# Performance work log

Hardware: AMD Instinct MI355X
Metric: run time of the kernel (lower is better)

## Reference

```python
import jax, jax.numpy as jnp
import numpy as np
import math

B, N, D = 64, 512, 300
MASK_VALUE = -1.0e9
LN_EPS = 1e-5


def setup_inputs() -> dict:
    key = jax.random.key(0)
    ks = jax.random.split(key, 8)
    return {
        "concepts": jax.random.normal(ks[0], (B, N, D), dtype=jnp.float32),
        "ocr_tokens": jax.random.normal(ks[1], (B, N, D), dtype=jnp.float32),
        "ocr_mask": jax.random.randint(ks[2], (B, N, 1), 0, 2, dtype=jnp.int32),
        "wq": jax.random.normal(ks[3], (D, D), dtype=jnp.float32) * (1.0 / math.sqrt(D)),
        "bq": jax.random.normal(ks[4], (D,), dtype=jnp.float32) * 0.02,
        "wk": jax.random.normal(ks[5], (D, D), dtype=jnp.float32) * (1.0 / math.sqrt(D)),
        "bk": jax.random.normal(ks[6], (D,), dtype=jnp.float32) * 0.02,
        "ln_w": jnp.ones((D,), dtype=jnp.float32),
        "ln_b": jnp.zeros((D,), dtype=jnp.float32),
    }


def _layer_norm(x, w, b):
    mu = jnp.mean(x, axis=-1, keepdims=True)
    var = jnp.mean(jnp.square(x - mu), axis=-1, keepdims=True)
    return (x - mu) * jax.lax.rsqrt(var + LN_EPS) * w + b


def reference(concepts, ocr_tokens, ocr_mask, wq, bq, wk, bk, ln_w, ln_b):
    # Q/K linear projections (torch Linear: x @ W^T + b)
    Q = jnp.einsum('bnd,ed->bne', concepts, wq) + bq      # [B,N,D]
    K = jnp.einsum('bmd,ed->bme', ocr_tokens, wk) + bk    # [B,N,D]
    # scaled attention scores over concepts x ocr tokens
    A = jnp.einsum('bne,bme->bnm', Q, K) / math.sqrt(D)   # [B,N,N]
    P = jax.nn.softmax(A, axis=-1)
    semantic = jnp.einsum('bnm,bmd->bnd', P, concepts)    # [B,N,D]
    # post-attention masked_fill (faithful to original: fill AFTER attention)
    semantic = jnp.where(ocr_mask == 0, jnp.float32(MASK_VALUE), semantic)
    out = _layer_norm(ocr_tokens + semantic, ln_w, ln_b)  # [B,N,D]
    return out
```

## Files before the change

kernel.cpp:

```cpp
#include <hip/hip_runtime.h>
#include <math.h>

#define Bb 64
#define Nn 512
#define Dd 300

typedef __attribute__((ext_vector_type(8))) short bfrag;
typedef __attribute__((ext_vector_type(4))) float f4;
typedef __attribute__((ext_vector_type(4))) unsigned u4;
typedef __attribute__((ext_vector_type(2))) unsigned u2;

union BF { unsigned u[4]; bfrag v; u4 q; };

__device__ inline unsigned bfr(float x){
    union{float f;unsigned u;}v; v.f=x;
    return (v.u + 0x7FFFu + ((v.u>>16)&1u))>>16;
}
__device__ inline unsigned pk_rne(float a, float b){ return bfr(a) | (bfr(b)<<16); }
__device__ inline unsigned pk_tr(float a, float b){
    union{float f;unsigned u;} ua, ub; ua.f=a; ub.f=b;
    return (ua.u>>16) | (ub.u & 0xFFFF0000u);
}
__device__ inline char* wadr(char* dout, unsigned f){
    return dout + (size_t)(f>>9)*1200u + 608u + (f&511u);
}
__device__ inline void async16(const char* g, char* l){
    __builtin_amdgcn_global_load_lds(
        (const __attribute__((address_space(1))) void*)g,
        (__attribute__((address_space(3))) void*)l, 16, 0, 0);
}

#define TSZ 38400
#define VOFF 19200
#define ZSZ 19200

__global__ __launch_bounds__(256)
void prep(const float* __restrict__ concepts, char* __restrict__ tiles,
          const float* __restrict__ wq, const float* __restrict__ wk,
          char* __restrict__ dout)
{
    const int bx = blockIdx.x;
    const int t  = threadIdx.x;
    if (bx < 1024) {
        const int mt = bx & 15, b = bx >> 4;
        char* vz = tiles + ((size_t)(b*16 + mt))*TSZ + VOFF;
        for (int task = t; task < 300; task += 256) {
            int m8 = task / 75, d4 = task - m8*75;
            const float* src = concepts + ((size_t)(b*Nn + mt*32 + m8*8))*Dd + d4*4;
            float4 r[8];
            #pragma unroll
            for (int i = 0; i < 8; ++i) r[i] = *(const float4*)(src + (size_t)i*Dd);
            #pragma unroll
            for (int dd = 0; dd < 4; ++dd) {
                int d = d4*4 + dd;
                float x[8];
                #pragma unroll
                for (int i = 0; i < 8; ++i)
                    x[i] = (dd==0) ? r[i].x : (dd==1) ? r[i].y : (dd==2) ? r[i].z : r[i].w;
                u4 q; q.x = pk_rne(x[0],x[1]); q.y = pk_rne(x[2],x[3]);
                      q.z = pk_rne(x[4],x[5]); q.w = pk_rne(x[6],x[7]);
                char* dst = (d < 288)
                    ? vz + (d>>4)*1024 + m8*256 + (d&15)*16
                    : vz + 18432 + m8*192 + (d-288)*16;
                *(u4*)dst = q;
            }
        }
    } else {
        const int wid = bx - 1024;
        const int xx = wid % 20, yy = wid / 20;
        const int sel = xx / 10, kc = xx % 10;
        const float* W = sel ? wk : wq;
        const int n = yy*152 + t;
        if (t < 152 && n < 304) {
            unsigned uu[16];
            #pragma unroll
            for (int j = 0; j < 16; ++j) uu[j] = 0;
            if (n < Dd) {
                const float* wr = W + (size_t)n*Dd + kc*32;
                int nv4 = (kc < 9) ? 8 : 3;
                #pragma unroll
                for (int i = 0; i < 8; ++i) {
                    if (i < nv4) {
                        float4 v = *(const float4*)(wr + i*4);
                        uu[2*i  ] = pk_rne(v.x, v.y);
                        uu[2*i+1] = pk_rne(v.z, v.w);
                    }
                }
            }
            unsigned fb = (unsigned)(sel*194560 + kc*19456 + n*16);
            #pragma unroll
            for (int g = 0; g < 4; ++g) {
                u4 q; q.x = uu[4*g+0]; q.y = uu[4*g+1]; q.z = uu[4*g+2]; q.w = uu[4*g+3];
                *(u4*)wadr(dout, fb + g*4864) = q;
            }
        }
    }
}

__global__ __launch_bounds__(256)
void proj4(const float* __restrict__ concepts, const float* __restrict__ ocr,
           const float* __restrict__ bq, const float* __restrict__ bk,
           char* __restrict__ dout, char* __restrict__ tiles)
{
    __shared__ char Wl[2][19456];
    const int t = threadIdx.x;
    const int w = t >> 6, lane = t & 63, ln = lane & 15, quad = lane >> 4;
    const int sel = blockIdx.y;
    const float* X    = sel ? ocr : concepts;
    const float* bias = sel ? bk  : bq;
    const int r0w = blockIdx.x*64 + w*16;
    const float* xr = X + (size_t)(r0w + ln)*Dd;

    const unsigned selbase = (unsigned)sel*194560u;
    #define STAGE_W(buf, kc) \
        for (int c = w; c < 19; c += 4) \
            async16((const char*)wadr(dout, selbase + (unsigned)(kc)*19456u + c*1024u + lane*16u), \
                    &Wl[buf][c*1024 + lane*16]);

    f4 acc[19];
    #pragma unroll
    for (int i = 0; i < 19; ++i) acc[i] = (f4){0.f,0.f,0.f,0.f};

    STAGE_W(0, 0);
    __syncthreads();

    for (int kc = 0; kc < 10; ++kc) {
        const int cur = kc & 1;
        if (kc < 9) { STAGE_W(1 - cur, kc + 1); }
        BF a;
        if (kc < 9) {
            float4 v0 = *(const float4*)(xr + kc*32 + quad*8);
            float4 v1 = *(const float4*)(xr + kc*32 + quad*8 + 4);
            a.u[0]=pk_tr(v0.x,v0.y); a.u[1]=pk_tr(v0.z,v0.w);
            a.u[2]=pk_tr(v1.x,v1.y); a.u[3]=pk_tr(v1.z,v1.w);
        } else {
            a.u[0]=0; a.u[1]=0; a.u[2]=0; a.u[3]=0;
            if (quad == 0) {
                float4 v0 = *(const float4*)(xr + 288);
                float4 v1 = *(const float4*)(xr + 292);
                a.u[0]=pk_tr(v0.x,v0.y); a.u[1]=pk_tr(v0.z,v0.w);
                a.u[2]=pk_tr(v1.x,v1.y); a.u[3]=pk_tr(v1.z,v1.w);
            } else if (quad == 1) {
                float4 v0 = *(const float4*)(xr + 296);
                a.u[0]=pk_tr(v0.x,v0.y); a.u[1]=pk_tr(v0.z,v0.w);
            }
        }
        #pragma unroll
        for (int nt = 0; nt < 19; ++nt) {
            BF bfv; bfv.q = *(const u4*)&Wl[cur][quad*4864 + nt*256 + ln*16];
            acc[nt] = __builtin_amdgcn_mfma_f32_16x16x32_bf16(a.v, bfv.v, acc[nt], 0,0,0);
        }
        __syncthreads();
    }

    const float QSCALE = 0.057735026918962584f;
    #pragma unroll
    for (int nt = 0; nt < 19; ++nt) {
        int e = nt*16 + ln;
        if (sel == 0) {
            #pragma unroll
            for (int reg = 0; reg < 4; ++reg) {
                int r = r0w + quad*4 + reg;
                short val = (e < Dd) ? (short)bfr((acc[nt][reg] + bias[e])*QSCALE) : (short)0;
                *(short*)(dout + (size_t)r*1200 + e*2) = val;
            }
        } else if (e < Dd) {
            float bv = bias[e];
            #pragma unroll
            for (int reg = 0; reg < 4; ++reg) {
                int r = r0w + quad*4 + reg;
                int b = r >> 9, m = r & 511, mt = m >> 5, ml = m & 31;
                char* tile = tiles + ((size_t)(b*16 + mt))*TSZ;
                short val = (short)bfr(acc[nt][reg] + bv);
                if (e < 288)
                    *(short*)(tile + 768 + (e>>5)*2048 + ((e>>3)&3)*512 + ml*16 + (e&7)*2) = val;
                else
                    *(short*)(tile + ml*24 + (e-288)*2) = val;
            }
        }
    }
}

__global__ __launch_bounds__(256)
void attn6(char* __restrict__ dout, const char* __restrict__ tiles,
           const float* __restrict__ ocr, const int* __restrict__ mask,
           const float* __restrict__ lnw, const float* __restrict__ lnb)
{
    __shared__ __align__(16) char Kb0[ZSZ];
    __shared__ __align__(16) char Kb1[ZSZ];
    __shared__ __align__(16) char Vb[ZSZ];
    const int t = threadIdx.x;
    const int w = t >> 6, lane = t & 63, ln = lane & 15, quad = lane >> 4;
    const int b = blockIdx.x, n0 = blockIdx.y*64;
    const int nlane = n0 + w*16 + ln;

    const char* qb = dout + (size_t)(b*Nn + nlane)*1200;
    bfrag qf[10];
    #pragma unroll
    for (int kc = 0; kc < 9; ++kc)
        qf[kc] = *(const bfrag*)(qb + kc*64 + quad*16);
    {
        BF z; z.u[0]=z.u[1]=z.u[2]=z.u[3]=0;
        if (quad < 2) z.q = *(const u4*)(qb + 576 + quad*16);
        qf[9] = z.v;
    }

    f4 oacc[19];
    #pragma unroll
    for (int i = 0; i < 19; ++i) oacc[i] = (f4){0.f,0.f,0.f,0.f};
    float lrun = 0.f;
    const char* tb = tiles + (size_t)b*16*TSZ;

#define STAGE_ZONE(SRC, DST) do { \
        const char* s_ = (SRC); char* d_ = (DST); \
        for (int c = w; c < 19; c += 4) \
            if (c < 18 || lane < 48) \
                async16(s_ + c*1024 + lane*16, d_ + c*1024 + lane*16); \
    } while (0)

    STAGE_ZONE(tb, Kb0);
    __syncthreads();

    auto step = [&](int mt, const char* Kz, char* Kw) {
        STAGE_ZONE(tb + (size_t)mt*TSZ + VOFF, Vb);

        f4 slo = (f4){0.f,0.f,0.f,0.f}, shi = (f4){0.f,0.f,0.f,0.f};
        __builtin_amdgcn_s_setprio(1);
        #pragma unroll
        for (int kc = 0; kc < 9; ++kc) {
            bfrag alo = *(const bfrag*)(Kz + 768 + kc*2048 + quad*512 + ln*16);
            bfrag ahi = *(const bfrag*)(Kz + 768 + kc*2048 + quad*512 + 256 + ln*16);
            slo = __builtin_amdgcn_mfma_f32_16x16x32_bf16(alo, qf[kc], slo, 0,0,0);
            shi = __builtin_amdgcn_mfma_f32_16x16x32_bf16(ahi, qf[kc], shi, 0,0,0);
        }
        {
            BF alo, ahi;
            alo.u[0]=alo.u[1]=alo.u[2]=alo.u[3]=0;
            ahi.u[0]=ahi.u[1]=ahi.u[2]=ahi.u[3]=0;
            if (quad < 2) {
                u2 x0 = *(const u2*)(Kz + ln*24 + quad*16);
                u2 x1 = *(const u2*)(Kz + ln*24 + quad*16 + 8);
                alo.u[0]=x0.x; alo.u[1]=x0.y; alo.u[2]=x1.x; alo.u[3]=x1.y;
                u2 y0 = *(const u2*)(Kz + (16+ln)*24 + quad*16);
                u2 y1 = *(const u2*)(Kz + (16+ln)*24 + quad*16 + 8);
                ahi.u[0]=y0.x; ahi.u[1]=y0.y; ahi.u[2]=y1.x; ahi.u[3]=y1.y;
            }
            slo = __builtin_amdgcn_mfma_f32_16x16x32_bf16(alo.v, qf[9], slo, 0,0,0);
            shi = __builtin_amdgcn_mfma_f32_16x16x32_bf16(ahi.v, qf[9], shi, 0,0,0);
        }
        __builtin_amdgcn_s_setprio(0);

        float elo[4], ehi[4], ls = 0.f;
        #pragma unroll
        for (int reg = 0; reg < 4; ++reg) {
            elo[reg] = __expf(slo[reg]);
            ehi[reg] = __expf(shi[reg]);
            ls += elo[reg] + ehi[reg];
        }
        ls += __shfl_xor(ls, 16);
        ls += __shfl_xor(ls, 32);
        lrun += ls;

        unsigned lo01 = pk_rne(elo[0], elo[1]), lo23 = pk_rne(elo[2], elo[3]);
        unsigned hi01 = pk_rne(ehi[0], ehi[1]), hi23 = pk_rne(ehi[2], ehi[3]);
        int sA = 2*(quad & 1)*16 + ln, sB = sA + 16;
        unsigned l0 = (unsigned)__shfl((int)lo01, sA);
        unsigned l1 = (unsigned)__shfl((int)lo23, sA);
        unsigned l2 = (unsigned)__shfl((int)lo01, sB);
        unsigned l3 = (unsigned)__shfl((int)lo23, sB);
        unsigned h0 = (unsigned)__shfl((int)hi01, sA);
        unsigned h1 = (unsigned)__shfl((int)hi23, sA);
        unsigned h2 = (unsigned)__shfl((int)hi01, sB);
        unsigned h3 = (unsigned)__shfl((int)hi23, sB);
        BF p;
        bool useHi = quad >= 2;
        p.u[0] = useHi ? h0 : l0; p.u[1] = useHi ? h1 : l1;
        p.u[2] = useHi ? h2 : l2; p.u[3] = useHi ? h3 : l3;

        __syncthreads();

        if (mt < 15) STAGE_ZONE(tb + (size_t)(mt+1)*TSZ, Kw);

        __builtin_amdgcn_s_setprio(1);
        #pragma unroll
        for (int nt = 0; nt < 18; ++nt) {
            bfrag vf = *(const bfrag*)(Vb + nt*1024 + lane*16);
            oacc[nt] = __builtin_amdgcn_mfma_f32_16x16x32_bf16(p.v, vf, oacc[nt], 0,0,0);
        }
        {
            BF vf; vf.u[0]=vf.u[1]=vf.u[2]=vf.u[3]=0;
            if (ln < 12) vf.q = *(const u4*)(Vb + 18432 + quad*192 + ln*16);
            oacc[18] = __builtin_amdgcn_mfma_f32_16x16x32_bf16(p.v, vf.v, oacc[18], 0,0,0);
        }
        __builtin_amdgcn_s_setprio(0);

        __syncthreads();
    };

    for (int mt2 = 0; mt2 < 16; mt2 += 2) {
        step(mt2,     Kb0, Kb1);
        step(mt2 + 1, Kb1, Kb0);
    }

    float invl[4];
    #pragma unroll
    for (int reg = 0; reg < 4; ++reg) invl[reg] = 1.0f / __shfl(lrun, quad*4 + reg);
    #pragma unroll
    for (int reg = 0; reg < 4; ++reg) {
        int r = b*Nn + n0 + w*16 + quad*4 + reg;
        int mr = mask[r];
        float xs[19], s = 0.f, ss = 0.f;
        #pragma unroll
        for (int nt = 0; nt < 19; ++nt) {
            int d = nt*16 + ln;
            float x = 0.f;
            if (d < Dd) x = oacc[nt][reg]*invl[reg] + ocr[(size_t)r*Dd + d];
            xs[nt] = x; s += x; ss += x*x;
        }
        #pragma unroll
        for (int off = 1; off < 16; off <<= 1) {
            s += __shfl_xor(s, off); ss += __shfl_xor(ss, off);
        }
        float mu   = s * (1.0f/Dd);
        float var  = ss * (1.0f/Dd) - mu*mu;
        float rstd = rsqrtf(var + 1e-5f);
        #pragma unroll
        for (int nt = 0; nt < 19; ++nt) {
            int d = nt*16 + ln;
            if (d < Dd) {
                float y = mr ? (xs[nt]-mu)*rstd*lnw[d] + lnb[d] : lnw[d] + lnb[d];
                *(float*)(dout + (size_t)r*1200 + d*4) = y;
            }
        }
    }
}

extern "C" void kernel_launch(void* const* d_in, const int* in_sizes, int n_in,
                              void* d_out, int out_size, void* d_ws, size_t ws_size,
                              hipStream_t stream)
{
    const float* concepts = (const float*)d_in[0];
    const float* ocr      = (const float*)d_in[1];
    const int*   mask     = (const int*)d_in[2];
    const float* wq  = (const float*)d_in[3];
    const float* bq  = (const float*)d_in[4];
    const float* wk  = (const float*)d_in[5];
    const float* bk  = (const float*)d_in[6];
    const float* lnw = (const float*)d_in[7];
    const float* lnb = (const float*)d_in[8];

    char* dout  = (char*)d_out;
    char* tiles = (char*)d_ws;

    prep <<<dim3(1064),    256, 0, stream>>>(concepts, tiles, wq, wk, dout);
    proj4<<<dim3(512, 2),  256, 0, stream>>>(concepts, ocr, bq, bk, dout, tiles);
    attn6<<<dim3(64, 8),   256, 0, stream>>>(dout, tiles, ocr, mask, lnw, lnb);
}
```

Before: 231.9 us.

## Load V fragments directly from global into registers, drop V LDS buffer

The attention kernel no longer stages V tiles into shared memory. Each lane loads its V fragments straight from global memory into registers at the start of each step. The K prefetch for the next tile is issued earlier, and one of the two barriers per step is removed. This reduces LDS footprint and synchronisation, and the launch bounds request two blocks per CU; the cost is higher register pressure (19 extra 16-byte fragments per lane) and exposed global-load latency before the PV MFMAs.

```diff
diff --git a/kernel.cpp b/kernel.cpp
--- a/kernel.cpp
+++ b/kernel.cpp
@@ -181,14 +181,12 @@
     }
 }
 
-__global__ __launch_bounds__(256)
-void attn6(char* __restrict__ dout, const char* __restrict__ tiles,
+__global__ __launch_bounds__(256, 2)
+void attn7(char* __restrict__ dout, const char* __restrict__ tiles,
            const float* __restrict__ ocr, const int* __restrict__ mask,
            const float* __restrict__ lnw, const float* __restrict__ lnb)
 {
-    __shared__ __align__(16) char Kb0[ZSZ];
-    __shared__ __align__(16) char Kb1[ZSZ];
-    __shared__ __align__(16) char Vb[ZSZ];
+    __shared__ __align__(16) char Kb[2][ZSZ];
     const int t = threadIdx.x;
     const int w = t >> 6, lane = t & 63, ln = lane & 15, quad = lane >> 4;
     const int b = blockIdx.x, n0 = blockIdx.y*64;
@@ -218,11 +216,24 @@
                 async16(s_ + c*1024 + lane*16, d_ + c*1024 + lane*16); \
     } while (0)
 
-    STAGE_ZONE(tb, Kb0);
+    STAGE_ZONE(tb, Kb[0]);
     __syncthreads();
 
-    auto step = [&](int mt, const char* Kz, char* Kw) {
-        STAGE_ZONE(tb + (size_t)mt*TSZ + VOFF, Vb);
+    for (int mt = 0; mt < 16; ++mt) {
+        const char* Kz = Kb[mt & 1];
+        char*       Kw = Kb[1 - (mt & 1)];
+        const char* Vg = tb + (size_t)mt*TSZ + VOFF;
+
+        BF vf[19];
+        #pragma unroll
+        for (int nt = 0; nt < 18; ++nt)
+            vf[nt].q = *(const u4*)(Vg + nt*1024 + lane*16);
+        {
+            vf[18].u[0]=0; vf[18].u[1]=0; vf[18].u[2]=0; vf[18].u[3]=0;
+            if (ln < 12) vf[18].q = *(const u4*)(Vg + 18432 + quad*192 + ln*16);
+        }
+
+        if (mt < 15) STAGE_ZONE(tb + (size_t)(mt+1)*TSZ, Kw);
 
         f4 slo = (f4){0.f,0.f,0.f,0.f}, shi = (f4){0.f,0.f,0.f,0.f};
         __builtin_amdgcn_s_setprio(1);
@@ -277,29 +288,13 @@
         p.u[0] = useHi ? h0 : l0; p.u[1] = useHi ? h1 : l1;
         p.u[2] = useHi ? h2 : l2; p.u[3] = useHi ? h3 : l3;
 
+        __builtin_amdgcn_s_setprio(1);
+        #pragma unroll
+        for (int nt = 0; nt < 19; ++nt)
+            oacc[nt] = __builtin_amdgcn_mfma_f32_16x16x32_bf16(p.v, vf[nt].v, oacc[nt], 0,0,0);
+        __builtin_amdgcn_s_setprio(0);
+
         __syncthreads();
-
-        if (mt < 15) STAGE_ZONE(tb + (size_t)(mt+1)*TSZ, Kw);
-
-        __builtin_amdgcn_s_setprio(1);
-        #pragma unroll
-        for (int nt = 0; nt < 18; ++nt) {
-            bfrag vf = *(const bfrag*)(Vb + nt*1024 + lane*16);
-            oacc[nt] = __builtin_amdgcn_mfma_f32_16x16x32_bf16(p.v, vf, oacc[nt], 0,0,0);
-        }
-        {
-            BF vf; vf.u[0]=vf.u[1]=vf.u[2]=vf.u[3]=0;
-            if (ln < 12) vf.q = *(const u4*)(Vb + 18432 + quad*192 + ln*16);
-            oacc[18] = __builtin_amdgcn_mfma_f32_16x16x32_bf16(p.v, vf.v, oacc[18], 0,0,0);
-        }
-        __builtin_amdgcn_s_setprio(0);
-
-        __syncthreads();
-    };
-
-    for (int mt2 = 0; mt2 < 16; mt2 += 2) {
-        step(mt2,     Kb0, Kb1);
-        step(mt2 + 1, Kb1, Kb0);
     }
 
     float invl[4];
@@ -354,5 +349,5 @@
 
     prep <<<dim3(1064),    256, 0, stream>>>(concepts, tiles, wq, wk, dout);
     proj4<<<dim3(512, 2),  256, 0, stream>>>(concepts, ocr, bq, bk, dout, tiles);
-    attn6<<<dim3(64, 8),   256, 0, stream>>>(dout, tiles, ocr, mask, lnw, lnb);
-}
+    attn7<<<dim3(64, 8),   256, 0, stream>>>(dout, tiles, ocr, mask, lnw, lnb);
+}
```

Measured after the change: 228.2 us. Within noise of the previous version (-1.6%).

## Double-buffer full K/V tiles with 512-thread blocks covering 128 query rows

Applied to the files above, without the earlier changes.

The attention kernel now uses 8 waves per block, each block handling 128 query rows instead of 64, so every staged K/V tile is reused by twice as many rows. Whole K+V tiles are double-buffered in LDS: the next tile is prefetched at the start of each step, which removes the separate V staging and one barrier per step. LDS per block grows to about 77 KB and the grid is halved to 256 blocks, so occupancy and the number of blocks per CU change. V loads are no longer hidden behind a mid-step barrier but are overlapped with a full step of compute.

```diff
diff --git a/kernel.cpp b/kernel.cpp
--- a/kernel.cpp
+++ b/kernel.cpp
@@ -32,7 +32,6 @@
 
 #define TSZ 38400
 #define VOFF 19200
-#define ZSZ 19200
 
 __global__ __launch_bounds__(256)
 void prep(const float* __restrict__ concepts, char* __restrict__ tiles,
@@ -181,17 +180,15 @@
     }
 }
 
-__global__ __launch_bounds__(256)
-void attn6(char* __restrict__ dout, const char* __restrict__ tiles,
+__global__ __launch_bounds__(512, 2)
+void attn8(char* __restrict__ dout, const char* __restrict__ tiles,
            const float* __restrict__ ocr, const int* __restrict__ mask,
            const float* __restrict__ lnw, const float* __restrict__ lnb)
 {
-    __shared__ __align__(16) char Kb0[ZSZ];
-    __shared__ __align__(16) char Kb1[ZSZ];
-    __shared__ __align__(16) char Vb[ZSZ];
+    __shared__ __align__(16) char Tb[2][TSZ];
     const int t = threadIdx.x;
     const int w = t >> 6, lane = t & 63, ln = lane & 15, quad = lane >> 4;
-    const int b = blockIdx.x, n0 = blockIdx.y*64;
+    const int b = blockIdx.x, n0 = blockIdx.y*128;
     const int nlane = n0 + w*16 + ln;
 
     const char* qb = dout + (size_t)(b*Nn + nlane)*1200;
@@ -211,18 +208,21 @@
     float lrun = 0.f;
     const char* tb = tiles + (size_t)b*16*TSZ;
 
-#define STAGE_ZONE(SRC, DST) do { \
+#define STAGE_TILE(SRC, DST) do { \
         const char* s_ = (SRC); char* d_ = (DST); \
-        for (int c = w; c < 19; c += 4) \
-            if (c < 18 || lane < 48) \
+        for (int c = w; c < 38; c += 8) \
+            if (c < 37 || lane < 32) \
                 async16(s_ + c*1024 + lane*16, d_ + c*1024 + lane*16); \
     } while (0)
 
-    STAGE_ZONE(tb, Kb0);
+    STAGE_TILE(tb, Tb[0]);
     __syncthreads();
 
-    auto step = [&](int mt, const char* Kz, char* Kw) {
-        STAGE_ZONE(tb + (size_t)mt*TSZ + VOFF, Vb);
+    for (int mt = 0; mt < 16; ++mt) {
+        const char* Kz = Tb[mt & 1];
+        const char* Vz = Kz + VOFF;
+
+        if (mt < 15) STAGE_TILE(tb + (size_t)(mt+1)*TSZ, Tb[1 - (mt & 1)]);
 
         f4 slo = (f4){0.f,0.f,0.f,0.f}, shi = (f4){0.f,0.f,0.f,0.f};
         __builtin_amdgcn_s_setprio(1);
@@ -277,29 +277,20 @@
         p.u[0] = useHi ? h0 : l0; p.u[1] = useHi ? h1 : l1;
         p.u[2] = useHi ? h2 : l2; p.u[3] = useHi ? h3 : l3;
 
-        __syncthreads();
-
-        if (mt < 15) STAGE_ZONE(tb + (size_t)(mt+1)*TSZ, Kw);
-
         __builtin_amdgcn_s_setprio(1);
         #pragma unroll
         for (int nt = 0; nt < 18; ++nt) {
-            bfrag vf = *(const bfrag*)(Vb + nt*1024 + lane*16);
+            bfrag vf = *(const bfrag*)(Vz + nt*1024 + lane*16);
             oacc[nt] = __builtin_amdgcn_mfma_f32_16x16x32_bf16(p.v, vf, oacc[nt], 0,0,0);
         }
         {
             BF vf; vf.u[0]=vf.u[1]=vf.u[2]=vf.u[3]=0;
-            if (ln < 12) vf.q = *(const u4*)(Vb + 18432 + quad*192 + ln*16);
+            if (ln < 12) vf.q = *(const u4*)(Vz + 18432 + quad*192 + ln*16);
             oacc[18] = __builtin_amdgcn_mfma_f32_16x16x32_bf16(p.v, vf.v, oacc[18], 0,0,0);
         }
         __builtin_amdgcn_s_setprio(0);
 
         __syncthreads();
-    };
-
-    for (int mt2 = 0; mt2 < 16; mt2 += 2) {
-        step(mt2,     Kb0, Kb1);
-        step(mt2 + 1, Kb1, Kb0);
     }
 
     float invl[4];
@@ -354,5 +345,5 @@
 
     prep <<<dim3(1064),    256, 0, stream>>>(concepts, tiles, wq, wk, dout);
     proj4<<<dim3(512, 2),  256, 0, stream>>>(concepts, ocr, bq, bk, dout, tiles);
-    attn6<<<dim3(64, 8),   256, 0, stream>>>(dout, tiles, ocr, mask, lnw, lnb);
-}
+    attn8<<<dim3(64, 4),   512, 0, stream>>>(dout, tiles, ocr, mask, lnw, lnb);
+}
```

Measured after the change: 226.9 us. 1.02x faster.
